# Kernel optimization log

Hardware: AMD Instinct MI355X
Metric: run time of the kernel (lower is better)

## Reference

```python
import jax, jax.numpy as jnp
import numpy as np


def setup_inputs() -> dict:
    key = jax.random.key(0)
    ks = jax.random.split(key, 5)
    B, S, D, H = 2, 2048, 1024, 16
    dk = D // H
    scale = D ** -0.5
    x = jax.random.normal(ks[0], (B, S, D), dtype=jnp.float32)
    W_Q = scale * jax.random.normal(ks[1], (H, D, dk), dtype=jnp.float32)
    W_K = scale * jax.random.normal(ks[2], (H, D, dk), dtype=jnp.float32)
    W_V = scale * jax.random.normal(ks[3], (H, D, dk), dtype=jnp.float32)
    W_O = scale * jax.random.normal(ks[4], (H * dk, D), dtype=jnp.float32)
    return {"x": x, "W_Q": W_Q, "W_K": W_K, "W_V": W_V, "W_O": W_O}


def reference(x, W_Q, W_K, W_V, W_O):
    # x: [B,S,D]; W_Q/W_K/W_V: [H,D,dk]; W_O: [H*dk, D]
    dk = W_Q.shape[-1]
    Q = jnp.einsum('bsd,hdk->bhsk', x, W_Q)
    K = jnp.einsum('bsd,hdk->bhsk', x, W_K)
    V = jnp.einsum('bsd,hdk->bhsk', x, W_V)
    scores = jnp.einsum('bhqk,bhsk->bhqs', Q, K) / jnp.sqrt(jnp.float32(dk))
    attn = jax.nn.softmax(scores, axis=-1)
    heads = jnp.einsum('bhqs,bhsk->bhqk', attn, V)  # [B,H,S,dk]
    B, H, S, _ = heads.shape
    concat = heads.transpose(0, 2, 1, 3).reshape(B, S, H * dk)  # [B,S,H*dk]
    return concat @ W_O
```

## Files before the change

kernel.cpp:

```cpp
#include <hip/hip_runtime.h>

typedef __attribute__((ext_vector_type(8))) short bf16x8;
typedef __attribute__((ext_vector_type(4))) float f32x4;
typedef __attribute__((ext_vector_type(4))) unsigned short u16x4;
typedef unsigned short u16;
typedef unsigned int u32;

static __device__ __forceinline__ u16 f2bf(float f) {
  u32 u = __float_as_uint(f);
  u32 r = (u + 0x7fffu + ((u >> 16) & 1u)) >> 16;
  return (u16)r;
}

static __device__ __forceinline__ u32 cvt_pk(float lo, float hi) {
  u32 r;
  asm("v_cvt_pk_bf16_f32 %0, %1, %2" : "=v"(r) : "v"(lo), "v"(hi));
  return r;
}

#define GLDS16(g, l)                                                        \
  __builtin_amdgcn_global_load_lds(                                         \
      (const __attribute__((address_space(1))) u32*)(g),                    \
      (__attribute__((address_space(3))) u32*)(l), 16, 0, 0)

#define WAIT_VM5() asm volatile("s_waitcnt vmcnt(5)" ::: "memory")
#define WAIT_VM8() asm volatile("s_waitcnt vmcnt(8)" ::: "memory")
#define WAIT_VM4() asm volatile("s_waitcnt vmcnt(4)" ::: "memory")
#define WAIT_VM0() asm volatile("s_waitcnt vmcnt(0)" ::: "memory")
#define RAWBAR() __builtin_amdgcn_s_barrier()

#define SC2F 0.18033688011112042f

__global__ __launch_bounds__(256) void cast_all(const float* __restrict__ x,
                                                const float* __restrict__ wq,
                                                const float* __restrict__ wk,
                                                const float* __restrict__ wv,
                                                const float* __restrict__ wo,
                                                u16* __restrict__ xb,
                                                u16* __restrict__ wqkv,
                                                u16* __restrict__ wot) {
  __shared__ u16 tile[64][66];
  int bid = blockIdx.x, t = threadIdx.x;
  if (bid < 2048) {
    int i = bid * 256 + t;
    const float4* xv = (const float4*)x;
    float4 a = xv[i * 2], b = xv[i * 2 + 1];
    bf16x8 o;
    o[0] = f2bf(a.x); o[1] = f2bf(a.y); o[2] = f2bf(a.z); o[3] = f2bf(a.w);
    o[4] = f2bf(b.x); o[5] = f2bf(b.y); o[6] = f2bf(b.z); o[7] = f2bf(b.w);
    *(bf16x8*)(xb + i * 8) = o;
    return;
  }
  const float* src;
  u16* dstb;
  if (bid < 2816) {
    int id = bid - 2048;
    int dt = id & 15, h = (id >> 4) & 15, sel = id >> 8;
    src = (sel == 0 ? wq : (sel == 1 ? wk : wv)) + h * 65536 + dt * 4096;
    dstb = wqkv + ((size_t)(h * 192 + sel * 64)) * 1024 + dt * 64;
    int r = t >> 4, c4 = (t & 15) * 4;
#pragma unroll
    for (int p = 0; p < 4; ++p) {
      int rr = r + p * 16;
      float4 v = *(const float4*)(src + rr * 64 + c4);
      u16x4 o;
      o[0] = f2bf(v.x); o[1] = f2bf(v.y); o[2] = f2bf(v.z); o[3] = f2bf(v.w);
      *(u16x4*)&tile[rr][c4] = o;
    }
  } else {
    int id = bid - 2816;
    int nt = id & 15, kt = id >> 4;
    src = wo + (size_t)(kt * 64) * 1024 + nt * 64;
    dstb = wot + (size_t)(nt * 64) * 1024 + kt * 64;
    int r = t >> 4, c4 = (t & 15) * 4;
#pragma unroll
    for (int p = 0; p < 4; ++p) {
      int rr = r + p * 16;
      float4 v = *(const float4*)(src + (size_t)rr * 1024 + c4);
      u16x4 o;
      o[0] = f2bf(v.x); o[1] = f2bf(v.y); o[2] = f2bf(v.z); o[3] = f2bf(v.w);
      *(u16x4*)&tile[rr][c4] = o;
    }
  }
  __syncthreads();
  int nn = t >> 3, dc = (t & 7) * 8;
#pragma unroll
  for (int p = 0; p < 2; ++p) {
    int np = nn + p * 32;
    u16x4 a, b2;
#pragma unroll
    for (int i = 0; i < 4; ++i) {
      a[i] = tile[dc + i][np];
      b2[i] = tile[dc + 4 + i][np];
    }
    *(u16x4*)(dstb + (size_t)np * 1024 + dc) = a;
    *(u16x4*)(dstb + (size_t)np * 1024 + dc + 4) = b2;
  }
}

__global__ __launch_bounds__(256) void gemm_qkv(const u16* __restrict__ A,
                                                const u16* __restrict__ Bt,
                                                u16* __restrict__ qkb,
                                                u16* __restrict__ Vt, int M,
                                                int N, int K) {
  const int t = threadIdx.x;
  const int lane = t & 63, w = t >> 6;
  const int lr = lane & 15, lg = lane >> 4;
  const int wr = w >> 1, wc = w & 1;
  int lin = blockIdx.y * gridDim.x + blockIdx.x;
  int nwg = gridDim.x * gridDim.y;
  int swz = (lin & 7) * (nwg >> 3) + (lin >> 3);
  int bx = swz % gridDim.x, by = swz / gridDim.x;
  const int m0 = by * 128, n0 = bx * 192, head = bx;
  __shared__ __align__(16) u16 SM[20480];
  const int ra = t >> 2, ca = (t & 3) * 8;
  const u16* a0 = A + (size_t)(m0 + ra) * K + ca;
  const u16* b0 = Bt + (size_t)(n0 + ra) * K + ca;
  f32x4 acc[4][6] = {};

#define QSTAGE(bb, k0)                                              \
  {                                                                 \
    GLDS16(a0 + (k0), &SM[(bb)*4096 + t * 8]);                      \
    GLDS16(a0 + (size_t)64 * K + (k0), &SM[(bb)*4096 + 2048 + t * 8]); \
    GLDS16(b0 + (k0), &SM[8192 + (bb)*6144 + t * 8]);               \
    GLDS16(b0 + (size_t)64 * K + (k0), &SM[8192 + (bb)*6144 + 2048 + t * 8]); \
    GLDS16(b0 + (size_t)128 * K + (k0), &SM[8192 + (bb)*6144 + 4096 + t * 8]); \
  }

  QSTAGE(0, 0);
  for (int k0 = 0; k0 < K; k0 += 32) {
    const int bb = (k0 >> 5) & 1;
    if (k0 + 32 < K) {
      QSTAGE(bb ^ 1, k0 + 32);
      WAIT_VM5();
    } else {
      WAIT_VM0();
    }
    RAWBAR();
    bf16x8 a[4], b[6];
#pragma unroll
    for (int m = 0; m < 4; ++m)
      a[m] = *(const bf16x8*)&SM[bb * 4096 + (wr * 64 + m * 16 + lr) * 32 + lg * 8];
#pragma unroll
    for (int n = 0; n < 6; ++n)
      b[n] = *(const bf16x8*)&SM[8192 + bb * 6144 + (wc * 96 + n * 16 + lr) * 32 + lg * 8];
    __builtin_amdgcn_s_setprio(1);
#pragma unroll
    for (int m = 0; m < 4; ++m)
#pragma unroll
      for (int n = 0; n < 6; ++n)
        acc[m][n] =
            __builtin_amdgcn_mfma_f32_16x16x32_bf16(a[m], b[n], acc[m][n], 0, 0, 0);
    __builtin_amdgcn_s_setprio(0);
    RAWBAR();
  }
#undef QSTAGE

#pragma unroll
  for (int m = 0; m < 4; ++m) {
    int rowg = m0 + wr * 64 + m * 16 + lg * 4;
#pragma unroll
    for (int n = 0; n < 6; ++n) {
      int cg = wc * 96 + n * 16 + lr;
      if (cg < 64) {
        int col = head * 64 + cg;
#pragma unroll
        for (int j = 0; j < 4; ++j)
          qkb[(size_t)(rowg + j) * 2048 + col] = f2bf(acc[m][n][j] * SC2F);
      } else if (cg < 128) {
        int col = 1024 + head * 64 + (cg - 64);
#pragma unroll
        for (int j = 0; j < 4; ++j)
          qkb[(size_t)(rowg + j) * 2048 + col] = f2bf(acc[m][n][j]);
      }
    }
  }
  __syncthreads();
  if (wc == 1) {
#pragma unroll
    for (int m = 0; m < 4; ++m)
#pragma unroll
      for (int n = 2; n < 6; ++n) {
        int v = (n - 2) * 16 + lr;
        int s = wr * 64 + m * 16 + lg * 4;
        u16x4 pk;
#pragma unroll
        for (int j = 0; j < 4; ++j) pk[j] = f2bf(acc[m][n][j]);
        *(u16x4*)&SM[v * 136 + s] = pk;
      }
  }
  __syncthreads();
  const int bb2 = m0 >> 11, s0g = m0 & 2047;
  u16* vdst = Vt + ((size_t)(bb2 * 1024 + head * 64)) * 2048 + s0g;
#pragma unroll
  for (int q = 0; q < 4; ++q) {
    int id = q * 256 + t;
    int v = id >> 4, sc = id & 15;
    bf16x8 row = *(const bf16x8*)&SM[v * 136 + sc * 8];
    *(bf16x8*)(vdst + (size_t)v * 2048 + sc * 8) = row;
  }
}

__global__ __launch_bounds__(256) void gemm_out(const u16* __restrict__ A,
                                                const u16* __restrict__ Bt,
                                                float* __restrict__ C, int M,
                                                int N, int K) {
  const int t = threadIdx.x;
  const int lane = t & 63, w = t >> 6;
  const int lr = lane & 15, lg = lane >> 4;
  const int wr = w >> 1, wc = w & 1;
  int lin = blockIdx.y * gridDim.x + blockIdx.x;
  int nwg = gridDim.x * gridDim.y;
  int swz = (lin & 7) * (nwg >> 3) + (lin >> 3);
  int bx = swz % gridDim.x, by = swz / gridDim.x;
  const int m0 = by * 128, n0 = bx * 128;
  __shared__ __align__(16) u16 As[2][128 * 32];
  __shared__ __align__(16) u16 Bs[2][128 * 32];
  const int r0 = t >> 2, cb = (t & 3) * 8;
  const u16* a0 = A + (size_t)(m0 + r0) * K + cb;
  const u16* b0 = Bt + (size_t)(n0 + r0) * K + cb;
  const size_t rowjmp = (size_t)64 * K;
  f32x4 acc[4][4] = {};

#define GSTAGE(bb, k0)                                      \
  {                                                         \
    GLDS16(a0 + (k0), &As[bb][t * 8]);                      \
    GLDS16(a0 + rowjmp + (k0), &As[bb][2048 + t * 8]);      \
    GLDS16(b0 + (k0), &Bs[bb][t * 8]);                      \
    GLDS16(b0 + rowjmp + (k0), &Bs[bb][2048 + t * 8]);      \
  }

  GSTAGE(0, 0);
  for (int k0 = 0; k0 < K; k0 += 32) {
    const int bb = (k0 >> 5) & 1;
    if (k0 + 32 < K) {
      GSTAGE(bb ^ 1, k0 + 32);
      WAIT_VM4();
    } else {
      WAIT_VM0();
    }
    RAWBAR();
    bf16x8 a[4], b[4];
#pragma unroll
    for (int m = 0; m < 4; ++m)
      a[m] = *(const bf16x8*)&As[bb][(wr * 64 + m * 16 + lr) * 32 + lg * 8];
#pragma unroll
    for (int n = 0; n < 4; ++n)
      b[n] = *(const bf16x8*)&Bs[bb][(wc * 64 + n * 16 + lr) * 32 + lg * 8];
    __builtin_amdgcn_s_setprio(1);
#pragma unroll
    for (int m = 0; m < 4; ++m)
#pragma unroll
      for (int n = 0; n < 4; ++n)
        acc[m][n] =
            __builtin_amdgcn_mfma_f32_16x16x32_bf16(a[m], b[n], acc[m][n], 0, 0, 0);
    __builtin_amdgcn_s_setprio(0);
    RAWBAR();
  }
#undef GSTAGE

#pragma unroll
  for (int m = 0; m < 4; ++m) {
    int rowg = m0 + wr * 64 + m * 16 + lg * 4;
#pragma unroll
    for (int n = 0; n < 4; ++n) {
      int colg = n0 + wc * 64 + n * 16 + lr;
#pragma unroll
      for (int j = 0; j < 4; ++j)
        C[(size_t)(rowg + j) * N + colg] = acc[m][n][j];
    }
  }
}

__global__ __launch_bounds__(256, 2) void attn(const u16* __restrict__ qkb,
                                               const u16* __restrict__ vtb,
                                               u16* __restrict__ hb) {
  const int t = threadIdx.x, lane = t & 63, w = t >> 6;
  const int lr = lane & 15, lg = lane >> 4;
  int lin = blockIdx.x;
  int swz2 = (lin & 7) * 64 + (lin >> 3);
  int qi = swz2 & 15, bh = swz2 >> 4;
  int b = bh >> 4, h = bh & 15;
  int q0 = qi * 128;
  __shared__ __align__(16) u16 Ks[2][128 * 64];
  __shared__ __align__(16) u16 Vts[2][64 * 128];
  __shared__ __align__(16) u32 Ps[4][2][512];

  bf16x8 qf[2][2];
#pragma unroll
  for (int g = 0; g < 2; ++g) {
    const u16* qb =
        qkb + (size_t)(b * 2048 + q0 + w * 32 + g * 16 + lr) * 2048 + h * 64;
    qf[g][0] = *(const bf16x8*)(qb + lg * 8);
    qf[g][1] = *(const bf16x8*)(qb + 32 + lg * 8);
  }

  f32x4 oacc[2][4] = {};
  float mrun0 = -1e30f, mrun1 = -1e30f;
  float lrun0 = 0.f, lrun1 = 0.f;

  int chk[2], chv[4];
#pragma unroll
  for (int kk = 0; kk < 2; ++kk) chk[kk] = ((kk * 4 + lg) ^ (lr & 7)) * 8;
#pragma unroll
  for (int kk = 0; kk < 4; ++kk) chv[kk] = ((kk * 4 + lg) ^ lr) * 8;
  const int xw = (lr & 7) << 2;

  const int rk = t >> 3, ck = t & 7;
  const int rv = t >> 4, cv = t & 15;
  const u16* Kg = qkb + (size_t)(b * 2048) * 2048 + 1024 + h * 64;
  const u16* Vg = vtb + (size_t)(b * 1024 + h * 64) * 2048;
  const u16* kp0 = Kg + (size_t)rk * 2048 + ((ck ^ (rk & 7)) * 8);
  const u16* vp0 = Vg + (size_t)rv * 2048 + ((cv ^ (rv & 15)) * 8);
  u32* Pw0 = &Ps[w][0][0];
  u32* Pw1 = &Ps[w][1][0];

#define ASTAGE(bb, tv)                                 \
  {                                                    \
    const u16* kp = kp0 + (size_t)(tv)*262144;         \
    const u16* vp = vp0 + (tv)*128;                    \
    GLDS16(kp, &Ks[bb][t * 8]);                        \
    GLDS16(kp + 65536, &Ks[bb][2048 + t * 8]);         \
    GLDS16(kp + 131072, &Ks[bb][4096 + t * 8]);        \
    GLDS16(kp + 196608, &Ks[bb][6144 + t * 8]);        \
    GLDS16(vp, &Vts[bb][t * 8]);                       \
    GLDS16(vp + 32768, &Vts[bb][2048 + t * 8]);        \
    GLDS16(vp + 65536, &Vts[bb][4096 + t * 8]);        \
    GLDS16(vp + 98304, &Vts[bb][6144 + t * 8]);        \
  }

  ASTAGE(0, 0);
  for (int tv = 0; tv < 16; ++tv) {
    const int bb = tv & 1;
    if (tv < 15) {
      ASTAGE(bb ^ 1, tv + 1);
      WAIT_VM8();
    } else {
      WAIT_VM0();
    }
    RAWBAR();

    f32x4 s0[8], s1[8];
#pragma unroll
    for (int n = 0; n < 8; ++n) {
      s0[n] = (f32x4){0.f, 0.f, 0.f, 0.f};
      s1[n] = (f32x4){0.f, 0.f, 0.f, 0.f};
    }
    __builtin_amdgcn_s_setprio(1);
#pragma unroll
    for (int kk = 0; kk < 2; ++kk)
#pragma unroll
      for (int n = 0; n < 8; ++n) {
        bf16x8 kf = *(const bf16x8*)&Ks[bb][n * 1024 + lr * 64 + chk[kk]];
        s0[n] = __builtin_amdgcn_mfma_f32_16x16x32_bf16(kf, qf[0][kk], s0[n], 0, 0, 0);
        s1[n] = __builtin_amdgcn_mfma_f32_16x16x32_bf16(kf, qf[1][kk], s1[n], 0, 0, 0);
      }
    __builtin_amdgcn_s_setprio(0);

    float t0[8], t1[8];
#pragma unroll
    for (int n = 0; n < 8; ++n) {
      t0[n] = fmaxf(fmaxf(s0[n][0], s0[n][1]), fmaxf(s0[n][2], s0[n][3]));
      t1[n] = fmaxf(fmaxf(s1[n][0], s1[n][1]), fmaxf(s1[n][2], s1[n][3]));
    }
    float pm0 = fmaxf(fmaxf(fmaxf(t0[0], t0[1]), fmaxf(t0[2], t0[3])),
                      fmaxf(fmaxf(t0[4], t0[5]), fmaxf(t0[6], t0[7])));
    float pm1 = fmaxf(fmaxf(fmaxf(t1[0], t1[1]), fmaxf(t1[2], t1[3])),
                      fmaxf(fmaxf(t1[4], t1[5]), fmaxf(t1[6], t1[7])));
    pm0 = fmaxf(pm0, __shfl_xor(pm0, 16));
    pm0 = fmaxf(pm0, __shfl_xor(pm0, 32));
    pm1 = fmaxf(pm1, __shfl_xor(pm1, 16));
    pm1 = fmaxf(pm1, __shfl_xor(pm1, 32));

    if (__any(fmaxf(pm0 - mrun0, pm1 - mrun1) > 8.0f)) {
      {
        float mn = fmaxf(mrun0, pm0);
        float al = __builtin_amdgcn_exp2f(mrun0 - mn);
        lrun0 *= al;
        float alj[4];
#pragma unroll
        for (int j = 0; j < 4; ++j) alj[j] = __shfl(al, 4 * lg + j);
#pragma unroll
        for (int n = 0; n < 4; ++n)
#pragma unroll
          for (int j = 0; j < 4; ++j) oacc[0][n][j] *= alj[j];
        mrun0 = mn;
      }
      {
        float mn = fmaxf(mrun1, pm1);
        float al = __builtin_amdgcn_exp2f(mrun1 - mn);
        lrun1 *= al;
        float alj[4];
#pragma unroll
        for (int j = 0; j < 4; ++j) alj[j] = __shfl(al, 4 * lg + j);
#pragma unroll
        for (int n = 0; n < 4; ++n)
#pragma unroll
          for (int j = 0; j < 4; ++j) oacc[1][n][j] *= alj[j];
        mrun1 = mn;
      }
    }

    float ps0 = 0.f, ps1 = 0.f;
#pragma unroll
    for (int n = 0; n < 4; ++n) {
      float v0 = __builtin_amdgcn_exp2f(s0[n][0] - mrun0);
      float v1 = __builtin_amdgcn_exp2f(s0[n][1] - mrun0);
      float v2 = __builtin_amdgcn_exp2f(s0[n][2] - mrun0);
      float v3 = __builtin_amdgcn_exp2f(s0[n][3] - mrun0);
      ps0 += (v0 + v1) + (v2 + v3);
      Pw0[lr * 32 + ((8 * n + 2 * lg) ^ xw)] = cvt_pk(v0, v1);
      Pw0[lr * 32 + ((8 * n + 2 * lg + 1) ^ xw)] = cvt_pk(v2, v3);
      float u0 = __builtin_amdgcn_exp2f(s1[n][0] - mrun1);
      float u1 = __builtin_amdgcn_exp2f(s1[n][1] - mrun1);
      float u2 = __builtin_amdgcn_exp2f(s1[n][2] - mrun1);
      float u3 = __builtin_amdgcn_exp2f(s1[n][3] - mrun1);
      ps1 += (u0 + u1) + (u2 + u3);
      Pw1[lr * 32 + ((8 * n + 2 * lg) ^ xw)] = cvt_pk(u0, u1);
      Pw1[lr * 32 + ((8 * n + 2 * lg + 1) ^ xw)] = cvt_pk(u2, u3);
    }
    __builtin_amdgcn_s_setprio(1);
#pragma unroll
    for (int kk = 0; kk < 2; ++kk) {
      bf16x8 pa0 = *(const bf16x8*)&Pw0[lr * 32 + ((16 * kk + 4 * lg) ^ xw)];
      bf16x8 pa1 = *(const bf16x8*)&Pw1[lr * 32 + ((16 * kk + 4 * lg) ^ xw)];
#pragma unroll
      for (int n = 0; n < 4; ++n) {
        bf16x8 vf = *(const bf16x8*)&Vts[bb][n * 2048 + lr * 128 + chv[kk]];
        oacc[0][n] = __builtin_amdgcn_mfma_f32_16x16x32_bf16(pa0, vf, oacc[0][n], 0, 0, 0);
        oacc[1][n] = __builtin_amdgcn_mfma_f32_16x16x32_bf16(pa1, vf, oacc[1][n], 0, 0, 0);
      }
    }
    __builtin_amdgcn_s_setprio(0);
#pragma unroll
    for (int n = 4; n < 8; ++n) {
      float v0 = __builtin_amdgcn_exp2f(s0[n][0] - mrun0);
      float v1 = __builtin_amdgcn_exp2f(s0[n][1] - mrun0);
      float v2 = __builtin_amdgcn_exp2f(s0[n][2] - mrun0);
      float v3 = __builtin_amdgcn_exp2f(s0[n][3] - mrun0);
      ps0 += (v0 + v1) + (v2 + v3);
      Pw0[lr * 32 + ((8 * (n - 4) + 2 * lg) ^ xw)] = cvt_pk(v0, v1);
      Pw0[lr * 32 + ((8 * (n - 4) + 2 * lg + 1) ^ xw)] = cvt_pk(v2, v3);
      float u0 = __builtin_amdgcn_exp2f(s1[n][0] - mrun1);
      float u1 = __builtin_amdgcn_exp2f(s1[n][1] - mrun1);
      float u2 = __builtin_amdgcn_exp2f(s1[n][2] - mrun1);
      float u3 = __builtin_amdgcn_exp2f(s1[n][3] - mrun1);
      ps1 += (u0 + u1) + (u2 + u3);
      Pw1[lr * 32 + ((8 * (n - 4) + 2 * lg) ^ xw)] = cvt_pk(u0, u1);
      Pw1[lr * 32 + ((8 * (n - 4) + 2 * lg + 1) ^ xw)] = cvt_pk(u2, u3);
    }
    __builtin_amdgcn_s_setprio(1);
#pragma unroll
    for (int kk = 2; kk < 4; ++kk) {
      bf16x8 pa0 = *(const bf16x8*)&Pw0[lr * 32 + ((16 * (kk - 2) + 4 * lg) ^ xw)];
      bf16x8 pa1 = *(const bf16x8*)&Pw1[lr * 32 + ((16 * (kk - 2) + 4 * lg) ^ xw)];
#pragma unroll
      for (int n = 0; n < 4; ++n) {
        bf16x8 vf = *(const bf16x8*)&Vts[bb][n * 2048 + lr * 128 + chv[kk]];
        oacc[0][n] = __builtin_amdgcn_mfma_f32_16x16x32_bf16(pa0, vf, oacc[0][n], 0, 0, 0);
        oacc[1][n] = __builtin_amdgcn_mfma_f32_16x16x32_bf16(pa1, vf, oacc[1][n], 0, 0, 0);
      }
    }
    __builtin_amdgcn_s_setprio(0);
    lrun0 += ps0;
    lrun1 += ps1;
    RAWBAR();
  }
#undef ASTAGE

  lrun0 += __shfl_xor(lrun0, 16);
  lrun0 += __shfl_xor(lrun0, 32);
  lrun1 += __shfl_xor(lrun1, 16);
  lrun1 += __shfl_xor(lrun1, 32);
  float ri0 = __builtin_amdgcn_rcpf(lrun0);
  float ri1 = __builtin_amdgcn_rcpf(lrun1);
  float rj0[4], rj1[4];
#pragma unroll
  for (int j = 0; j < 4; ++j) {
    rj0[j] = __shfl(ri0, 4 * lg + j);
    rj1[j] = __shfl(ri1, 4 * lg + j);
  }
  int row0 = b * 2048 + q0 + w * 32 + lg * 4;
#pragma unroll
  for (int n = 0; n < 4; ++n) {
    int col = h * 64 + n * 16 + lr;
#pragma unroll
    for (int j = 0; j < 4; ++j) {
      hb[(size_t)(row0 + j) * 1024 + col] = f2bf(oacc[0][n][j] * rj0[j]);
      hb[(size_t)(row0 + 16 + j) * 1024 + col] = f2bf(oacc[1][n][j] * rj1[j]);
    }
  }
}

extern "C" void kernel_launch(void* const* d_in, const int* in_sizes, int n_in,
                              void* d_out, int out_size, void* d_ws,
                              size_t ws_size, hipStream_t stream) {
  const float* x = (const float*)d_in[0];
  const float* wq = (const float*)d_in[1];
  const float* wk = (const float*)d_in[2];
  const float* wv = (const float*)d_in[3];
  const float* wo = (const float*)d_in[4];

  u16* xb = (u16*)d_ws;
  u16* wqkv = xb + 4 * 1024 * 1024;
  u16* wot = wqkv + 3 * 1024 * 1024;
  u16* qkb = wot + 1024 * 1024;
  u16* vtb = qkb + 8 * 1024 * 1024;
  u16* hb = vtb + 4 * 1024 * 1024;

  cast_all<<<3072, 256, 0, stream>>>(x, wq, wk, wv, wo, xb, wqkv, wot);
  gemm_qkv<<<dim3(16, 32), 256, 0, stream>>>(xb, wqkv, qkb, vtb, 4096, 3072, 1024);
  attn<<<512, 256, 0, stream>>>(qkb, vtb, hb);
  gemm_out<<<dim3(8, 32), 256, 0, stream>>>(hb, wot, (float*)d_out, 4096, 1024, 1024);
}
```

Measured before the change: 123.3 us.

## Shrink output GEMM M-tile, compute softmax row sums via MFMA, use max3

The output GEMM tile shrinks from 128x128 to 64x128 and its grid doubles to 512 workgroups, giving more parallelism for a 4096x1024 output on many CUs. In attention, the per-row softmax denominator is now accumulated by an extra MFMA against a ones vector instead of scalar adds and end-of-loop shuffles. The row-max reduction uses v_max3_f32. The trade-offs are more MFMA work per tile, bf16-rounded P in the denominator, and less operand reuse per GEMM block.

```diff
diff --git a/kernel.cpp b/kernel.cpp
--- a/kernel.cpp
+++ b/kernel.cpp
@@ -18,6 +18,12 @@
   return r;
 }
 
+static __device__ __forceinline__ float max3(float a, float b, float c) {
+  float r;
+  asm("v_max3_f32 %0, %1, %2, %3" : "=v"(r) : "v"(a), "v"(b), "v"(c));
+  return r;
+}
+
 #define GLDS16(g, l)                                                        \
   __builtin_amdgcn_global_load_lds(                                         \
       (const __attribute__((address_space(1))) u32*)(g),                    \
@@ -25,7 +31,7 @@
 
 #define WAIT_VM5() asm volatile("s_waitcnt vmcnt(5)" ::: "memory")
 #define WAIT_VM8() asm volatile("s_waitcnt vmcnt(8)" ::: "memory")
-#define WAIT_VM4() asm volatile("s_waitcnt vmcnt(4)" ::: "memory")
+#define WAIT_VM3() asm volatile("s_waitcnt vmcnt(3)" ::: "memory")
 #define WAIT_VM0() asm volatile("s_waitcnt vmcnt(0)" ::: "memory")
 #define RAWBAR() __builtin_amdgcn_s_barrier()
 
@@ -213,19 +219,18 @@
   int nwg = gridDim.x * gridDim.y;
   int swz = (lin & 7) * (nwg >> 3) + (lin >> 3);
   int bx = swz % gridDim.x, by = swz / gridDim.x;
-  const int m0 = by * 128, n0 = bx * 128;
-  __shared__ __align__(16) u16 As[2][128 * 32];
+  const int m0 = by * 64, n0 = bx * 128;
+  __shared__ __align__(16) u16 As[2][64 * 32];
   __shared__ __align__(16) u16 Bs[2][128 * 32];
   const int r0 = t >> 2, cb = (t & 3) * 8;
   const u16* a0 = A + (size_t)(m0 + r0) * K + cb;
   const u16* b0 = Bt + (size_t)(n0 + r0) * K + cb;
   const size_t rowjmp = (size_t)64 * K;
-  f32x4 acc[4][4] = {};
+  f32x4 acc[2][4] = {};
 
 #define GSTAGE(bb, k0)                                      \
   {                                                         \
     GLDS16(a0 + (k0), &As[bb][t * 8]);                      \
-    GLDS16(a0 + rowjmp + (k0), &As[bb][2048 + t * 8]);      \
     GLDS16(b0 + (k0), &Bs[bb][t * 8]);                      \
     GLDS16(b0 + rowjmp + (k0), &Bs[bb][2048 + t * 8]);      \
   }
@@ -235,21 +240,21 @@
     const int bb = (k0 >> 5) & 1;
     if (k0 + 32 < K) {
       GSTAGE(bb ^ 1, k0 + 32);
-      WAIT_VM4();
+      WAIT_VM3();
     } else {
       WAIT_VM0();
     }
     RAWBAR();
-    bf16x8 a[4], b[4];
-#pragma unroll
-    for (int m = 0; m < 4; ++m)
-      a[m] = *(const bf16x8*)&As[bb][(wr * 64 + m * 16 + lr) * 32 + lg * 8];
+    bf16x8 a[2], b[4];
+#pragma unroll
+    for (int m = 0; m < 2; ++m)
+      a[m] = *(const bf16x8*)&As[bb][(wr * 32 + m * 16 + lr) * 32 + lg * 8];
 #pragma unroll
     for (int n = 0; n < 4; ++n)
       b[n] = *(const bf16x8*)&Bs[bb][(wc * 64 + n * 16 + lr) * 32 + lg * 8];
     __builtin_amdgcn_s_setprio(1);
 #pragma unroll
-    for (int m = 0; m < 4; ++m)
+    for (int m = 0; m < 2; ++m)
 #pragma unroll
       for (int n = 0; n < 4; ++n)
         acc[m][n] =
@@ -260,8 +265,8 @@
 #undef GSTAGE
 
 #pragma unroll
-  for (int m = 0; m < 4; ++m) {
-    int rowg = m0 + wr * 64 + m * 16 + lg * 4;
+  for (int m = 0; m < 2; ++m) {
+    int rowg = m0 + wr * 32 + m * 16 + lg * 4;
 #pragma unroll
     for (int n = 0; n < 4; ++n) {
       int colg = n0 + wc * 64 + n * 16 + lr;
@@ -294,10 +299,13 @@
     qf[g][0] = *(const bf16x8*)(qb + lg * 8);
     qf[g][1] = *(const bf16x8*)(qb + 32 + lg * 8);
   }
+  bf16x8 ones;
+#pragma unroll
+  for (int i = 0; i < 8; ++i) ones[i] = (short)0x3F80;
 
   f32x4 oacc[2][4] = {};
+  f32x4 le0 = {}, le1 = {};
   float mrun0 = -1e30f, mrun1 = -1e30f;
-  float lrun0 = 0.f, lrun1 = 0.f;
 
   int chk[2], chv[4];
 #pragma unroll
@@ -360,13 +368,13 @@
     float t0[8], t1[8];
 #pragma unroll
     for (int n = 0; n < 8; ++n) {
-      t0[n] = fmaxf(fmaxf(s0[n][0], s0[n][1]), fmaxf(s0[n][2], s0[n][3]));
-      t1[n] = fmaxf(fmaxf(s1[n][0], s1[n][1]), fmaxf(s1[n][2], s1[n][3]));
-    }
-    float pm0 = fmaxf(fmaxf(fmaxf(t0[0], t0[1]), fmaxf(t0[2], t0[3])),
-                      fmaxf(fmaxf(t0[4], t0[5]), fmaxf(t0[6], t0[7])));
-    float pm1 = fmaxf(fmaxf(fmaxf(t1[0], t1[1]), fmaxf(t1[2], t1[3])),
-                      fmaxf(fmaxf(t1[4], t1[5]), fmaxf(t1[6], t1[7])));
+      t0[n] = fmaxf(max3(s0[n][0], s0[n][1], s0[n][2]), s0[n][3]);
+      t1[n] = fmaxf(max3(s1[n][0], s1[n][1], s1[n][2]), s1[n][3]);
+    }
+    float pm0 = fmaxf(max3(max3(t0[0], t0[1], t0[2]), t0[3], t0[4]),
+                      max3(t0[5], t0[6], t0[7]));
+    float pm1 = fmaxf(max3(max3(t1[0], t1[1], t1[2]), t1[3], t1[4]),
+                      max3(t1[5], t1[6], t1[7]));
     pm0 = fmaxf(pm0, __shfl_xor(pm0, 16));
     pm0 = fmaxf(pm0, __shfl_xor(pm0, 32));
     pm1 = fmaxf(pm1, __shfl_xor(pm1, 16));
@@ -376,10 +384,11 @@
       {
         float mn = fmaxf(mrun0, pm0);
         float al = __builtin_amdgcn_exp2f(mrun0 - mn);
-        lrun0 *= al;
         float alj[4];
 #pragma unroll
         for (int j = 0; j < 4; ++j) alj[j] = __shfl(al, 4 * lg + j);
+#pragma unroll
+        for (int j = 0; j < 4; ++j) le0[j] *= alj[j];
 #pragma unroll
         for (int n = 0; n < 4; ++n)
 #pragma unroll
@@ -389,10 +398,11 @@
       {
         float mn = fmaxf(mrun1, pm1);
         float al = __builtin_amdgcn_exp2f(mrun1 - mn);
-        lrun1 *= al;
         float alj[4];
 #pragma unroll
         for (int j = 0; j < 4; ++j) alj[j] = __shfl(al, 4 * lg + j);
+#pragma unroll
+        for (int j = 0; j < 4; ++j) le1[j] *= alj[j];
 #pragma unroll
         for (int n = 0; n < 4; ++n)
 #pragma unroll
@@ -401,21 +411,18 @@
       }
     }
 
-    float ps0 = 0.f, ps1 = 0.f;
 #pragma unroll
     for (int n = 0; n < 4; ++n) {
       float v0 = __builtin_amdgcn_exp2f(s0[n][0] - mrun0);
       float v1 = __builtin_amdgcn_exp2f(s0[n][1] - mrun0);
       float v2 = __builtin_amdgcn_exp2f(s0[n][2] - mrun0);
       float v3 = __builtin_amdgcn_exp2f(s0[n][3] - mrun0);
-      ps0 += (v0 + v1) + (v2 + v3);
       Pw0[lr * 32 + ((8 * n + 2 * lg) ^ xw)] = cvt_pk(v0, v1);
       Pw0[lr * 32 + ((8 * n + 2 * lg + 1) ^ xw)] = cvt_pk(v2, v3);
       float u0 = __builtin_amdgcn_exp2f(s1[n][0] - mrun1);
       float u1 = __builtin_amdgcn_exp2f(s1[n][1] - mrun1);
       float u2 = __builtin_amdgcn_exp2f(s1[n][2] - mrun1);
       float u3 = __builtin_amdgcn_exp2f(s1[n][3] - mrun1);
-      ps1 += (u0 + u1) + (u2 + u3);
       Pw1[lr * 32 + ((8 * n + 2 * lg) ^ xw)] = cvt_pk(u0, u1);
       Pw1[lr * 32 + ((8 * n + 2 * lg + 1) ^ xw)] = cvt_pk(u2, u3);
     }
@@ -424,6 +431,8 @@
     for (int kk = 0; kk < 2; ++kk) {
       bf16x8 pa0 = *(const bf16x8*)&Pw0[lr * 32 + ((16 * kk + 4 * lg) ^ xw)];
       bf16x8 pa1 = *(const bf16x8*)&Pw1[lr * 32 + ((16 * kk + 4 * lg) ^ xw)];
+      le0 = __builtin_amdgcn_mfma_f32_16x16x32_bf16(pa0, ones, le0, 0, 0, 0);
+      le1 = __builtin_amdgcn_mfma_f32_16x16x32_bf16(pa1, ones, le1, 0, 0, 0);
 #pragma unroll
       for (int n = 0; n < 4; ++n) {
         bf16x8 vf = *(const bf16x8*)&Vts[bb][n * 2048 + lr * 128 + chv[kk]];
@@ -438,14 +447,12 @@
       float v1 = __builtin_amdgcn_exp2f(s0[n][1] - mrun0);
       float v2 = __builtin_amdgcn_exp2f(s0[n][2] - mrun0);
       float v3 = __builtin_amdgcn_exp2f(s0[n][3] - mrun0);
-      ps0 += (v0 + v1) + (v2 + v3);
       Pw0[lr * 32 + ((8 * (n - 4) + 2 * lg) ^ xw)] = cvt_pk(v0, v1);
       Pw0[lr * 32 + ((8 * (n - 4) + 2 * lg + 1) ^ xw)] = cvt_pk(v2, v3);
       float u0 = __builtin_amdgcn_exp2f(s1[n][0] - mrun1);
       float u1 = __builtin_amdgcn_exp2f(s1[n][1] - mrun1);
       float u2 = __builtin_amdgcn_exp2f(s1[n][2] - mrun1);
       float u3 = __builtin_amdgcn_exp2f(s1[n][3] - mrun1);
-      ps1 += (u0 + u1) + (u2 + u3);
       Pw1[lr * 32 + ((8 * (n - 4) + 2 * lg) ^ xw)] = cvt_pk(u0, u1);
       Pw1[lr * 32 + ((8 * (n - 4) + 2 * lg + 1) ^ xw)] = cvt_pk(u2, u3);
     }
@@ -454,6 +461,8 @@
     for (int kk = 2; kk < 4; ++kk) {
       bf16x8 pa0 = *(const bf16x8*)&Pw0[lr * 32 + ((16 * (kk - 2) + 4 * lg) ^ xw)];
       bf16x8 pa1 = *(const bf16x8*)&Pw1[lr * 32 + ((16 * (kk - 2) + 4 * lg) ^ xw)];
+      le0 = __builtin_amdgcn_mfma_f32_16x16x32_bf16(pa0, ones, le0, 0, 0, 0);
+      le1 = __builtin_amdgcn_mfma_f32_16x16x32_bf16(pa1, ones, le1, 0, 0, 0);
 #pragma unroll
       for (int n = 0; n < 4; ++n) {
         bf16x8 vf = *(const bf16x8*)&Vts[bb][n * 2048 + lr * 128 + chv[kk]];
@@ -462,23 +471,15 @@
       }
     }
     __builtin_amdgcn_s_setprio(0);
-    lrun0 += ps0;
-    lrun1 += ps1;
     RAWBAR();
   }
 #undef ASTAGE
 
-  lrun0 += __shfl_xor(lrun0, 16);
-  lrun0 += __shfl_xor(lrun0, 32);
-  lrun1 += __shfl_xor(lrun1, 16);
-  lrun1 += __shfl_xor(lrun1, 32);
-  float ri0 = __builtin_amdgcn_rcpf(lrun0);
-  float ri1 = __builtin_amdgcn_rcpf(lrun1);
   float rj0[4], rj1[4];
 #pragma unroll
   for (int j = 0; j < 4; ++j) {
-    rj0[j] = __shfl(ri0, 4 * lg + j);
-    rj1[j] = __shfl(ri1, 4 * lg + j);
+    rj0[j] = __builtin_amdgcn_rcpf(le0[j]);
+    rj1[j] = __builtin_amdgcn_rcpf(le1[j]);
   }
   int row0 = b * 2048 + q0 + w * 32 + lg * 4;
 #pragma unroll
@@ -511,5 +512,5 @@
   cast_all<<<3072, 256, 0, stream>>>(x, wq, wk, wv, wo, xb, wqkv, wot);
   gemm_qkv<<<dim3(16, 32), 256, 0, stream>>>(xb, wqkv, qkb, vtb, 4096, 3072, 1024);
   attn<<<512, 256, 0, stream>>>(qkb, vtb, hb);
-  gemm_out<<<dim3(8, 32), 256, 0, stream>>>(hb, wot, (float*)d_out, 4096, 1024, 1024);
-}
+  gemm_out<<<dim3(8, 64), 256, 0, stream>>>(hb, wot, (float*)d_out, 4096, 1024, 1024);
+}
```

Result: faster. 116.3 us (-5.7%).
